# Kernel optimization log

Hardware: AMD Instinct MI355X
Metric: run time of the kernel (lower is better)

Reference implementation:

```python
import jax, jax.numpy as jnp
import numpy as np

N, S, B, E = 32768, 1024, 32, 262144   # nodes, nodes-per-graph, graphs, edges
C, H, L = 128, 4, 4                    # hidden, heads, layers
ND, ED, PE = 64, 16, 16                # node_dim, edge_dim, pe_dim
DH = C // H
LN_EPS = 1e-5


def _mlp2(h, w1, b1, w2, b2, act=jax.nn.relu):
    # mlp(ch_in, ch_out, hidden, num_hidden_layers=1): Linear -> act -> Linear (dropout = identity at inference)
    return act(h @ w1 + b1) @ w2 + b2


def _layer_norm(h, g, b):
    mu = jnp.mean(h, axis=-1, keepdims=True)
    var = jnp.var(h, axis=-1, keepdims=True)
    return (h - mu) * jax.lax.rsqrt(var + LN_EPS) * g + b


def setup_inputs() -> dict:
    key = jax.random.key(0)
    ks = iter(jax.random.split(key, 64))
    def nrm(shape, scale=0.05):
        return jax.random.normal(next(ks), shape, jnp.float32) * scale
    x = jax.random.normal(next(ks), (N, ND), jnp.float32)
    lap_pe = jax.random.normal(next(ks), (N, PE), jnp.float32)
    edge_attr = jax.random.normal(next(ks), (E, ED), jnp.float32)
    # edges within graphs: each graph occupies a contiguous block of S nodes
    g = jax.random.randint(next(ks), (E,), 0, B)
    src = g * S + jax.random.randint(next(ks), (E,), 0, S)
    dst = g * S + jax.random.randint(next(ks), (E,), 0, S)
    edge_index = jnp.stack([src, dst]).astype(jnp.int32)
    batch = (jnp.arange(N) // S).astype(jnp.int32)
    inp = dict(x=x, edge_index=edge_index, batch=batch, edge_attr=edge_attr, lap_pe=lap_pe)
    inp.update(
        node_w1=nrm((ND + PE, C)), node_b1=jnp.zeros((C,)), node_w2=nrm((C, C)), node_b2=jnp.zeros((C,)),
        edge_w1=nrm((ED, C)), edge_b1=jnp.zeros((C,)), edge_w2=nrm((C, C)), edge_b2=jnp.zeros((C,)),
        eps=jnp.zeros((L,)),
        gin_w1=nrm((L, C, C)), gin_b1=jnp.zeros((L, C)), gin_w2=nrm((L, C, C)), gin_b2=jnp.zeros((L, C)),
        elin_w=nrm((L, C, C)), elin_b=jnp.zeros((L, C)),
        attn_qkv_w=nrm((L, C, 3 * C)), attn_qkv_b=jnp.zeros((L, 3 * C)),
        attn_out_w=nrm((L, C, C)), attn_out_b=jnp.zeros((L, C)),
        mlp_w1=nrm((L, C, 2 * C)), mlp_b1=jnp.zeros((L, 2 * C)),
        mlp_w2=nrm((L, 2 * C, C)), mlp_b2=jnp.zeros((L, C)),
        ln1_g=jnp.ones((L, C)), ln1_b=jnp.zeros((L, C)),
        ln2_g=jnp.ones((L, C)), ln2_b=jnp.zeros((L, C)),
        ln3_g=jnp.ones((L, C)), ln3_b=jnp.zeros((L, C)),
        post_w1=nrm((C, C)), post_b1=jnp.zeros((C,)), post_w2=nrm((C, C)), post_b2=jnp.zeros((C,)),
        ro_w1=nrm((C, C)), ro_b1=jnp.zeros((C,)), ro_w2=nrm((C, 1)), ro_b2=jnp.zeros((1,)),
    )
    return inp


def reference(x, edge_index, batch, edge_attr, lap_pe,
              node_w1, node_b1, node_w2, node_b2,
              edge_w1, edge_b1, edge_w2, edge_b2,
              eps, gin_w1, gin_b1, gin_w2, gin_b2, elin_w, elin_b,
              attn_qkv_w, attn_qkv_b, attn_out_w, attn_out_b,
              mlp_w1, mlp_b1, mlp_w2, mlp_b2,
              ln1_g, ln1_b, ln2_g, ln2_b, ln3_g, ln3_b,
              post_w1, post_b1, post_w2, post_b2,
              ro_w1, ro_b1, ro_w2, ro_b2):
    src, dst = edge_index[0], edge_index[1]
    x = jnp.concatenate([x, lap_pe], axis=-1)
    x = _mlp2(x, node_w1, node_b1, node_w2, node_b2)
    e = _mlp2(edge_attr, edge_w1, edge_b1, edge_w2, edge_b2)
    scale = 1.0 / np.sqrt(DH)
    for i in range(L):
        # --- local GINEConv: nn((1+eps)*x_i + sum_j relu(x_j + lin(e_ij))) ---
        m = jax.nn.relu(x[src] + e @ elin_w[i] + elin_b[i])           # [E, C]
        agg = jax.ops.segment_sum(m, dst, num_segments=N)             # [N, C]
        hl = _mlp2((1.0 + eps[i]) * x + agg, gin_w1[i], gin_b1[i], gin_w2[i], gin_b2[i])
        hl = _layer_norm(hl + x, ln1_g[i], ln1_b[i])
        # --- global multihead attention over dense per-graph batch (equal sizes => reshape) ---
        xd = x.reshape(B, S, C)
        q, k, v = jnp.split(xd @ attn_qkv_w[i] + attn_qkv_b[i], 3, axis=-1)
        q = q.reshape(B, S, H, DH).transpose(0, 2, 1, 3)              # [B,H,S,DH]
        k = k.reshape(B, S, H, DH).transpose(0, 2, 1, 3)
        v = v.reshape(B, S, H, DH).transpose(0, 2, 1, 3)
        att = jax.nn.softmax(jnp.einsum('bhqd,bhkd->bhqk', q, k) * scale, axis=-1)
        o = jnp.einsum('bhqk,bhkd->bhqd', att, v).transpose(0, 2, 1, 3).reshape(B, S, C)
        ha = (o @ attn_out_w[i] + attn_out_b[i]).reshape(N, C)
        ha = _layer_norm(ha + x, ln2_g[i], ln2_b[i])
        # --- combine + FFN (act='gelu') + norm3, then outer residual ---
        out = hl + ha
        out = out + _mlp2(out, mlp_w1[i], mlp_b1[i], mlp_w2[i], mlp_b2[i], act=jax.nn.gelu)
        h = _layer_norm(out, ln3_g[i], ln3_b[i])
        x = x + h
    x = x + _mlp2(x, post_w1, post_b1, post_w2, post_b2)
    sums = jax.ops.segment_sum(x, batch, num_segments=B)
    cnt = jax.ops.segment_sum(jnp.ones((N, 1), x.dtype), batch, num_segments=B)
    gmean = sums / cnt
    return _mlp2(gmean, ro_w1, ro_b1, ro_w2, ro_b2)                   # [B, 1]
```

## Files before the change

### kernel.cpp

```cpp
#include <hip/hip_runtime.h>
#include <math.h>

namespace {

constexpr int N_  = 32768;
constexpr int S_  = 1024;
constexpr int B_  = 32;
constexpr int E_  = 262144;
constexpr int C_  = 128;
constexpr int ND_ = 64;
constexpr int PE_ = 16;
constexpr int ED_ = 16;
constexpr float LNE = 1e-5f;

typedef __attribute__((ext_vector_type(8))) short short8;
typedef __attribute__((ext_vector_type(4))) float floatx4;

__device__ inline float gelu_tanh(float v) {
  const float c = 0.7978845608028654f;
  return 0.5f * v * (1.0f + tanhf(c * (v + 0.044715f * v * v * v)));
}

__device__ inline unsigned short f2bf_u(float f) {
  unsigned u = __float_as_uint(f);
  u += 0x7fff + ((u >> 16) & 1);
  return (unsigned short)(u >> 16);
}

__device__ inline float bf2f(unsigned short v) {
  return __uint_as_float(((unsigned)v) << 16);
}

__device__ inline float block_sum128(float v, float* red, int t) {
  red[t] = v;
  __syncthreads();
#pragma unroll
  for (int off = 64; off > 0; off >>= 1) {
    if (t < off) red[t] += red[t + off];
    __syncthreads();
  }
  float r = red[0];
  __syncthreads();
  return r;
}

__global__ void k_zero(float4* __restrict__ p, int n4) {
  int i = blockIdx.x * 256 + threadIdx.x;
  if (i < n4) p[i] = make_float4(0.f, 0.f, 0.f, 0.f);
}

__global__ void k_count(const int* __restrict__ dst, int* __restrict__ hist) {
  int e = blockIdx.x * 256 + threadIdx.x;
  if (e < E_) atomicAdd(&hist[dst[e]], 1);
}

__global__ __launch_bounds__(1024) void k_scan(int* __restrict__ hist, int* __restrict__ binStart) {
  __shared__ int sums[1024];
  int t = threadIdx.x;
  int base = t * 32;
  int loc[32];
  int s = 0;
#pragma unroll
  for (int i = 0; i < 32; ++i) { loc[i] = s; s += hist[base + i]; }
  sums[t] = s;
  __syncthreads();
  for (int off = 1; off < 1024; off <<= 1) {
    int v = (t >= off) ? sums[t - off] : 0;
    __syncthreads();
    sums[t] += v;
    __syncthreads();
  }
  int excl = sums[t] - s;
#pragma unroll
  for (int i = 0; i < 32; ++i) {
    int v = excl + loc[i];
    binStart[base + i] = v;
    hist[base + i] = v;
  }
  if (t == 1023) binStart[32768] = sums[1023];
}

__global__ void k_scatter(const int* __restrict__ dst, int* __restrict__ cursor,
                          int* __restrict__ perm) {
  int e = blockIdx.x * 256 + threadIdx.x;
  if (e < E_) {
    int p = atomicAdd(&cursor[dst[e]], 1);
    perm[p] = e;
  }
}

__global__ void k_gather_edges(const float* __restrict__ ea, const int* __restrict__ src,
                               const int* __restrict__ dst, const int* __restrict__ perm,
                               float* __restrict__ ea_s, int* __restrict__ src_s,
                               int* __restrict__ dst_s) {
  int p4 = blockIdx.x * 256 + threadIdx.x;
  int p = p4 >> 2, c4 = p4 & 3;
  int e = perm[p];
  ((float4*)(ea_s + (size_t)p * ED_))[c4] = ((const float4*)(ea + (size_t)e * ED_))[c4];
  if (c4 == 0) { src_s[p] = src[e]; dst_s[p] = dst[e]; }
}

__global__ void k_fuse_w(const float* __restrict__ w2, const float* __restrict__ b2,
                         const float* __restrict__ elin_w, const float* __restrict__ elin_b,
                         unsigned short* __restrict__ fw2t, float* __restrict__ fb2) {
  int t = threadIdx.x;
  int bid = blockIdx.x;
  int layer = bid / (C_ + 1);
  int k = bid % (C_ + 1);
  const float* el = elin_w + (size_t)layer * C_ * C_;
  if (k < C_) {
    float a = 0.0f;
    for (int m = 0; m < C_; ++m) a += w2[k * C_ + m] * el[m * C_ + t];
    fw2t[(size_t)layer * C_ * C_ + t * C_ + k] = f2bf_u(a);
  } else {
    float a = elin_b[layer * C_ + t];
    for (int m = 0; m < C_; ++m) a += b2[m] * el[m * C_ + t];
    fb2[layer * C_ + t] = a;
  }
}

__global__ void k_prep_ew1(const float* __restrict__ ew1, unsigned short* __restrict__ ew1t) {
  int n = blockIdx.x;
  int k = threadIdx.x;
  ew1t[n * 32 + k] = (k < ED_) ? f2bf_u(ew1[k * C_ + n]) : (unsigned short)0;
}

__global__ void k_prep(const float* __restrict__ gin_w1, const float* __restrict__ gin_w2,
                       const float* __restrict__ aqkv_w, const float* __restrict__ aout_w,
                       const float* __restrict__ mlp_w1, const float* __restrict__ mlp_w2,
                       unsigned short* __restrict__ wt) {
  int t = threadIdx.x;
  int bid = blockIdx.x;
  int l = bid / 1152;
  int r = bid % 1152;
  unsigned short* base = wt + (size_t)l * 163840;
  if (r < 128) {
    base[r * 128 + t] = f2bf_u(gin_w1[(size_t)l * 16384 + t * 128 + r]);
  } else if (r < 256) {
    int n = r - 128;
    base[16384 + n * 128 + t] = f2bf_u(gin_w2[(size_t)l * 16384 + t * 128 + n]);
  } else if (r < 640) {
    int n = r - 256;
    base[32768 + n * 128 + t] = f2bf_u(aqkv_w[(size_t)l * 49152 + t * 384 + n]);
  } else if (r < 768) {
    int n = r - 640;
    base[81920 + n * 128 + t] = f2bf_u(aout_w[(size_t)l * 16384 + t * 128 + n]);
  } else if (r < 1024) {
    int n = r - 768;
    base[98304 + n * 128 + t] = f2bf_u(mlp_w1[(size_t)l * 32768 + t * 256 + n]);
  } else {
    int n = r - 1024;
    base[131072 + n * 256 + t]       = f2bf_u(mlp_w2[(size_t)l * 32768 + t * 128 + n]);
    base[131072 + n * 256 + 128 + t] = f2bf_u(mlp_w2[(size_t)l * 32768 + (t + 128) * 128 + n]);
  }
}

__global__ void k_node_enc(const float* __restrict__ xin, const float* __restrict__ pe,
                           const float* __restrict__ w1, const float* __restrict__ b1,
                           const float* __restrict__ w2, const float* __restrict__ b2,
                           float* __restrict__ xout) {
  __shared__ float inL[4][80];
  __shared__ float hidL[4][C_];
  int t = threadIdx.x;
  int row0 = blockIdx.x * 4;
#pragma unroll
  for (int r = 0; r < 4; ++r) {
    int row = row0 + r;
    if (t < ND_) inL[r][t] = xin[(size_t)row * ND_ + t];
    else if (t < 80) inL[r][t] = pe[(size_t)row * PE_ + (t - ND_)];
  }
  __syncthreads();
  float acc[4];
  float bb = b1[t];
#pragma unroll
  for (int r = 0; r < 4; ++r) acc[r] = bb;
  for (int k = 0; k < 80; ++k) {
    float wv = w1[k * C_ + t];
#pragma unroll
    for (int r = 0; r < 4; ++r) acc[r] += inL[r][k] * wv;
  }
#pragma unroll
  for (int r = 0; r < 4; ++r) hidL[r][t] = fmaxf(acc[r], 0.0f);
  __syncthreads();
  float bb2 = b2[t];
#pragma unroll
  for (int r = 0; r < 4; ++r) acc[r] = bb2;
  for (int k = 0; k < C_; ++k) {
    float wv = w2[k * C_ + t];
#pragma unroll
    for (int r = 0; r < 4; ++r) acc[r] += hidL[r][k] * wv;
  }
#pragma unroll
  for (int r = 0; r < 4; ++r) xout[(size_t)(row0 + r) * C_ + t] = acc[r];
}

__global__ __launch_bounds__(256) void k_edge_mfma(
    const float* __restrict__ ea_s, const float* __restrict__ x,
    const int* __restrict__ src_s, const int* __restrict__ dst_s,
    const unsigned short* __restrict__ ew1t, const float* __restrict__ eb1,
    const unsigned short* __restrict__ fw2t, const float* __restrict__ fb2,
    float* __restrict__ agg) {
  __shared__ unsigned short eaL[64][40];
  __shared__ unsigned short buf[64][136];
  __shared__ int srcL[64], dstL[64];
  int tid = threadIdx.x;
  int e0 = blockIdx.x * 64;

  if (tid < 64) { srcL[tid] = src_s[e0 + tid]; dstL[tid] = dst_s[e0 + tid]; }
  {
    int r = tid >> 2, c4 = tid & 3;
    float4 v = ((const float4*)(ea_s + (size_t)(e0 + r) * ED_))[c4];
    ushort4 u;
    u.x = f2bf_u(v.x); u.y = f2bf_u(v.y); u.z = f2bf_u(v.z); u.w = f2bf_u(v.w);
    *(ushort4*)&eaL[r][c4 * 4] = u;
    ushort4 z4 = {0, 0, 0, 0};
    *(ushort4*)&eaL[r][16 + c4 * 4] = z4;
  }
  __syncthreads();

  int lane = tid & 63;
  int w = tid >> 6;
  int li = lane & 15;
  int quad = lane >> 4;
  int r0 = w * 16;

  short8 aE = *(const short8*)&eaL[r0 + li][quad * 8];
#pragma unroll
  for (int t8 = 0; t8 < 8; ++t8) {
    short8 bE = *(const short8*)(ew1t + (size_t)(t8 * 16 + li) * 32 + quad * 8);
    floatx4 z = {0.f, 0.f, 0.f, 0.f};
    floatx4 h = __builtin_amdgcn_mfma_f32_16x16x32_bf16(aE, bE, z, 0, 0, 0);
    float bv = eb1[t8 * 16 + li];
#pragma unroll
    for (int reg = 0; reg < 4; ++reg)
      buf[r0 + quad * 4 + reg][t8 * 16 + li] = f2bf_u(fmaxf(h[reg] + bv, 0.f));
  }
  __syncthreads();

  short8 aK[4];
#pragma unroll
  for (int k4 = 0; k4 < 4; ++k4)
    aK[k4] = *(const short8*)&buf[r0 + li][k4 * 32 + quad * 8];
  __syncthreads();

  float fbv[8];
#pragma unroll
  for (int t8 = 0; t8 < 8; ++t8) fbv[t8] = fb2[t8 * 16 + li];

#pragma unroll
  for (int t8 = 0; t8 < 8; ++t8) {
    floatx4 acc = {0.f, 0.f, 0.f, 0.f};
    const unsigned short* bp = fw2t + (size_t)(t8 * 16 + li) * C_ + quad * 8;
#pragma unroll
    for (int k4 = 0; k4 < 4; ++k4) {
      short8 bf = *(const short8*)(bp + k4 * 32);
      acc = __builtin_amdgcn_mfma_f32_16x16x32_bf16(aK[k4], bf, acc, 0, 0, 0);
    }
    int n = t8 * 16 + li;
#pragma unroll
    for (int reg = 0; reg < 4; ++reg) {
      int cr = r0 + quad * 4 + reg;
      float v = fmaxf(acc[reg] + fbv[t8] + x[(size_t)srcL[cr] * C_ + n], 0.0f);
      buf[cr][n] = f2bf_u(v);
    }
  }
  __syncthreads();

  {
    int col = tid & 127;
    int rbase = (tid >> 7) * 32;
    float run = bf2f(buf[rbase][col]);
    int cur = dstL[rbase];
    for (int r = 1; r < 32; ++r) {
      int rr = rbase + r;
      int d = dstL[rr];
      float v = bf2f(buf[rr][col]);
      if (d != cur) {
        atomicAdd(&agg[(size_t)cur * C_ + col], run);
        run = v; cur = d;
      } else {
        run += v;
      }
    }
    atomicAdd(&agg[(size_t)cur * C_ + col], run);
  }
}

__global__ __launch_bounds__(256) void k_gin_mfma(
    const float* __restrict__ x, const float* __restrict__ agg,
    const unsigned short* __restrict__ w1t, const float* __restrict__ b1,
    const unsigned short* __restrict__ w2t, const float* __restrict__ b2,
    const float* __restrict__ g, const float* __restrict__ bln,
    const float* __restrict__ epsarr, int layer, float* __restrict__ hl) {
  __shared__ unsigned short inL[64][136];
  __shared__ unsigned short hidL[64][136];
  int tid = threadIdx.x;
  int row0 = blockIdx.x * 64;
  float epsv = 1.0f + epsarr[layer];
#pragma unroll
  for (int i = 0; i < 8; ++i) {
    int p = i * 256 + tid;
    int r = p >> 5, c4 = p & 31;
    float4 xa = *(const float4*)(x + (size_t)(row0 + r) * C_ + c4 * 4);
    float4 ag = *(const float4*)(agg + (size_t)(row0 + r) * C_ + c4 * 4);
    ushort4 u;
    u.x = f2bf_u(epsv * xa.x + ag.x);
    u.y = f2bf_u(epsv * xa.y + ag.y);
    u.z = f2bf_u(epsv * xa.z + ag.z);
    u.w = f2bf_u(epsv * xa.w + ag.w);
    *(ushort4*)&inL[r][c4 * 4] = u;
  }
  __syncthreads();
  int lane = tid & 63, w = tid >> 6, li = lane & 15, quad = lane >> 4;
  int r0 = w * 16;

  short8 aK[4];
#pragma unroll
  for (int k4 = 0; k4 < 4; ++k4) aK[k4] = *(const short8*)&inL[r0 + li][k4 * 32 + quad * 8];
  floatx4 acc[8];
#pragma unroll
  for (int t8 = 0; t8 < 8; ++t8) acc[t8] = (floatx4){0.f, 0.f, 0.f, 0.f};
#pragma unroll
  for (int t8 = 0; t8 < 8; ++t8) {
    const unsigned short* bp = w1t + (size_t)(t8 * 16 + li) * 128 + quad * 8;
#pragma unroll
    for (int k4 = 0; k4 < 4; ++k4) {
      short8 bf = *(const short8*)(bp + k4 * 32);
      acc[t8] = __builtin_amdgcn_mfma_f32_16x16x32_bf16(aK[k4], bf, acc[t8], 0, 0, 0);
    }
  }
#pragma unroll
  for (int t8 = 0; t8 < 8; ++t8) {
    float bv = b1[t8 * 16 + li];
#pragma unroll
    for (int reg = 0; reg < 4; ++reg)
      hidL[r0 + quad * 4 + reg][t8 * 16 + li] = f2bf_u(fmaxf(acc[t8][reg] + bv, 0.f));
  }
  short8 aK2[4];
#pragma unroll
  for (int k4 = 0; k4 < 4; ++k4) aK2[k4] = *(const short8*)&hidL[r0 + li][k4 * 32 + quad * 8];
  floatx4 acc2[8];
#pragma unroll
  for (int t8 = 0; t8 < 8; ++t8) acc2[t8] = (floatx4){0.f, 0.f, 0.f, 0.f};
#pragma unroll
  for (int t8 = 0; t8 < 8; ++t8) {
    const unsigned short* bp = w2t + (size_t)(t8 * 16 + li) * 128 + quad * 8;
#pragma unroll
    for (int k4 = 0; k4 < 4; ++k4) {
      short8 bf = *(const short8*)(bp + k4 * 32);
      acc2[t8] = __builtin_amdgcn_mfma_f32_16x16x32_bf16(aK2[k4], bf, acc2[t8], 0, 0, 0);
    }
  }
  float gv[8], blv[8], b2v[8];
#pragma unroll
  for (int t8 = 0; t8 < 8; ++t8) {
    int col = t8 * 16 + li;
    gv[t8] = g[col]; blv[t8] = bln[col]; b2v[t8] = b2[col];
  }
#pragma unroll
  for (int reg = 0; reg < 4; ++reg) {
    int row = row0 + r0 + quad * 4 + reg;
    float v[8], s = 0.f, s2 = 0.f;
#pragma unroll
    for (int t8 = 0; t8 < 8; ++t8) {
      float xv = x[(size_t)row * C_ + t8 * 16 + li];
      v[t8] = acc2[t8][reg] + b2v[t8] + xv;
      s += v[t8]; s2 += v[t8] * v[t8];
    }
#pragma unroll
    for (int m = 1; m <= 8; m <<= 1) { s += __shfl_xor(s, m); s2 += __shfl_xor(s2, m); }
    float mu = s * (1.0f / C_);
    float var = s2 * (1.0f / C_) - mu * mu;
    float inv = rsqrtf(var + LNE);
#pragma unroll
    for (int t8 = 0; t8 < 8; ++t8)
      hl[(size_t)row * C_ + t8 * 16 + li] = (v[t8] - mu) * inv * gv[t8] + blv[t8];
  }
}

__global__ __launch_bounds__(256) void k_qkv_mfma(
    const float* __restrict__ x, const unsigned short* __restrict__ qkvt,
    const float* __restrict__ b, unsigned short* __restrict__ qkvb) {
  __shared__ unsigned short inL[64][136];
  int tid = threadIdx.x;
  int row0 = blockIdx.x * 64;
#pragma unroll
  for (int i = 0; i < 8; ++i) {
    int p = i * 256 + tid;
    int r = p >> 5, c4 = p & 31;
    float4 xa = *(const float4*)(x + (size_t)(row0 + r) * C_ + c4 * 4);
    ushort4 u;
    u.x = f2bf_u(xa.x); u.y = f2bf_u(xa.y); u.z = f2bf_u(xa.z); u.w = f2bf_u(xa.w);
    *(ushort4*)&inL[r][c4 * 4] = u;
  }
  __syncthreads();
  int lane = tid & 63, w = tid >> 6, li = lane & 15, quad = lane >> 4;
  int r0 = w * 16;
  short8 aK[4];
#pragma unroll
  for (int k4 = 0; k4 < 4; ++k4) aK[k4] = *(const short8*)&inL[r0 + li][k4 * 32 + quad * 8];
  floatx4 acc[24];
#pragma unroll
  for (int t8 = 0; t8 < 24; ++t8) acc[t8] = (floatx4){0.f, 0.f, 0.f, 0.f};
#pragma unroll
  for (int t8 = 0; t8 < 24; ++t8) {
    const unsigned short* bp = qkvt + (size_t)(t8 * 16 + li) * 128 + quad * 8;
#pragma unroll
    for (int k4 = 0; k4 < 4; ++k4) {
      short8 bf = *(const short8*)(bp + k4 * 32);
      acc[t8] = __builtin_amdgcn_mfma_f32_16x16x32_bf16(aK[k4], bf, acc[t8], 0, 0, 0);
    }
  }
#pragma unroll
  for (int t8 = 0; t8 < 24; ++t8) {
    int col = t8 * 16 + li;
    float bv = b[col];
#pragma unroll
    for (int reg = 0; reg < 4; ++reg) {
      int row = row0 + r0 + quad * 4 + reg;
      qkvb[(size_t)row * 384 + col] = f2bf_u(acc[t8][reg] + bv);
    }
  }
}

__global__ __launch_bounds__(256) void k_attn_mfma(const unsigned short* __restrict__ qkvb,
                                                   float* __restrict__ attno) {
  __shared__ unsigned short kL[2][32][40];
  __shared__ unsigned short vT[2][32][40];
  __shared__ unsigned short pL[4][16][40];
  int tid = threadIdx.x;
  int lane = tid & 63;
  int w = tid >> 6;
  int li = lane & 15;
  int quad = lane >> 4;
  int bid = blockIdx.x;
  int b = (bid & 7) * 4 + ((bid >> 3) & 3);
  int rest = bid >> 5;
  int h = rest & 3;
  int qt = rest >> 2;
  int qbase = b * S_ + qt * 64 + w * 16;

  short8 qA = *(const short8*)(qkvb + (size_t)(qbase + li) * 384 + h * 32 + quad * 8);

  floatx4 o0 = {0.f, 0.f, 0.f, 0.f}, o1 = {0.f, 0.f, 0.f, 0.f};
  float lsum[4] = {0.f, 0.f, 0.f, 0.f};
  const float scale = 0.17677669529663687f;

  int half = tid >> 7;
  int tt = tid & 127;
  int j = tt >> 2;
  int seg = tt & 3;
  int vcol = (((j >> 3) ^ seg) & 3) * 8 + (j & 7);
  int vg0 = ((quad ^ (li >> 3)) & 3) * 8;
  int vg1 = ((quad ^ (2 + (li >> 3))) & 3) * 8;

  for (int kc = 0; kc < 32; ++kc) {
    int buf = kc & 1;
    {
      int node = b * S_ + kc * 32 + j;
      const unsigned short* p = qkvb + (size_t)node * 384 + (half ? 256 : 128) + h * 32 + seg * 8;
      short8 val = *(const short8*)p;
      if (half == 0) {
        *(short8*)&kL[buf][j][seg * 8] = val;
      } else {
#pragma unroll
        for (int i = 0; i < 8; ++i) vT[buf][seg * 8 + i][vcol] = (unsigned short)val[i];
      }
    }
    __syncthreads();
    short8 kB0 = *(const short8*)&kL[buf][li][quad * 8];
    short8 kB1 = *(const short8*)&kL[buf][16 + li][quad * 8];
    floatx4 z = {0.f, 0.f, 0.f, 0.f};
    floatx4 s0 = __builtin_amdgcn_mfma_f32_16x16x32_bf16(qA, kB0, z, 0, 0, 0);
    floatx4 s1 = __builtin_amdgcn_mfma_f32_16x16x32_bf16(qA, kB1, z, 0, 0, 0);
#pragma unroll
    for (int r = 0; r < 4; ++r) {
      float p0 = __expf(s0[r] * scale);
      float p1 = __expf(s1[r] * scale);
      lsum[r] += p0 + p1;
      pL[w][quad * 4 + r][li] = f2bf_u(p0);
      pL[w][quad * 4 + r][16 + li] = f2bf_u(p1);
    }
    short8 pA  = *(const short8*)&pL[w][li][quad * 8];
    short8 vB0 = *(const short8*)&vT[buf][li][vg0];
    short8 vB1 = *(const short8*)&vT[buf][16 + li][vg1];
    o0 = __builtin_amdgcn_mfma_f32_16x16x32_bf16(pA, vB0, o0, 0, 0, 0);
    o1 = __builtin_amdgcn_mfma_f32_16x16x32_bf16(pA, vB1, o1, 0, 0, 0);
  }
#pragma unroll
  for (int r = 0; r < 4; ++r) {
    float l = lsum[r];
#pragma unroll
    for (int msk = 1; msk <= 8; msk <<= 1) l += __shfl_xor(l, msk);
    float inv = 1.0f / l;
    size_t row = (size_t)(qbase + quad * 4 + r);
    attno[row * C_ + h * 32 + li] = o0[r] * inv;
    attno[row * C_ + h * 32 + 16 + li] = o1[r] * inv;
  }
}

__global__ __launch_bounds__(256) void k_attnout_mfma(
    const float* __restrict__ attno, const float* __restrict__ x,
    const unsigned short* __restrict__ wt, const float* __restrict__ b,
    const float* __restrict__ g, const float* __restrict__ bln,
    float* __restrict__ ha) {
  __shared__ unsigned short inL[64][136];
  int tid = threadIdx.x;
  int row0 = blockIdx.x * 64;
#pragma unroll
  for (int i = 0; i < 8; ++i) {
    int p = i * 256 + tid;
    int r = p >> 5, c4 = p & 31;
    float4 xa = *(const float4*)(attno + (size_t)(row0 + r) * C_ + c4 * 4);
    ushort4 u;
    u.x = f2bf_u(xa.x); u.y = f2bf_u(xa.y); u.z = f2bf_u(xa.z); u.w = f2bf_u(xa.w);
    *(ushort4*)&inL[r][c4 * 4] = u;
  }
  __syncthreads();
  int lane = tid & 63, w = tid >> 6, li = lane & 15, quad = lane >> 4;
  int r0 = w * 16;
  short8 aK[4];
#pragma unroll
  for (int k4 = 0; k4 < 4; ++k4) aK[k4] = *(const short8*)&inL[r0 + li][k4 * 32 + quad * 8];
  floatx4 acc[8];
#pragma unroll
  for (int t8 = 0; t8 < 8; ++t8) acc[t8] = (floatx4){0.f, 0.f, 0.f, 0.f};
#pragma unroll
  for (int t8 = 0; t8 < 8; ++t8) {
    const unsigned short* bp = wt + (size_t)(t8 * 16 + li) * 128 + quad * 8;
#pragma unroll
    for (int k4 = 0; k4 < 4; ++k4) {
      short8 bf = *(const short8*)(bp + k4 * 32);
      acc[t8] = __builtin_amdgcn_mfma_f32_16x16x32_bf16(aK[k4], bf, acc[t8], 0, 0, 0);
    }
  }
  float gv[8], blv[8], bv[8];
#pragma unroll
  for (int t8 = 0; t8 < 8; ++t8) {
    int col = t8 * 16 + li;
    gv[t8] = g[col]; blv[t8] = bln[col]; bv[t8] = b[col];
  }
#pragma unroll
  for (int reg = 0; reg < 4; ++reg) {
    int row = row0 + r0 + quad * 4 + reg;
    float v[8], s = 0.f, s2 = 0.f;
#pragma unroll
    for (int t8 = 0; t8 < 8; ++t8) {
      float xv = x[(size_t)row * C_ + t8 * 16 + li];
      v[t8] = acc[t8][reg] + bv[t8] + xv;
      s += v[t8]; s2 += v[t8] * v[t8];
    }
#pragma unroll
    for (int m = 1; m <= 8; m <<= 1) { s += __shfl_xor(s, m); s2 += __shfl_xor(s2, m); }
    float mu = s * (1.0f / C_);
    float var = s2 * (1.0f / C_) - mu * mu;
    float inv = rsqrtf(var + LNE);
#pragma unroll
    for (int t8 = 0; t8 < 8; ++t8)
      ha[(size_t)row * C_ + t8 * 16 + li] = (v[t8] - mu) * inv * gv[t8] + blv[t8];
  }
}

__global__ __launch_bounds__(256) void k_ffn_mfma(
    const float* __restrict__ hl, const float* __restrict__ ha,
    float* __restrict__ x,
    const unsigned short* __restrict__ w1t, const float* __restrict__ b1,
    const unsigned short* __restrict__ w2t, const float* __restrict__ b2,
    const float* __restrict__ g, const float* __restrict__ bln) {
  __shared__ unsigned short inL[64][136];
  __shared__ unsigned short hidL[64][264];
  int tid = threadIdx.x;
  int row0 = blockIdx.x * 64;
#pragma unroll
  for (int i = 0; i < 8; ++i) {
    int p = i * 256 + tid;
    int r = p >> 5, c4 = p & 31;
    float4 a = *(const float4*)(hl + (size_t)(row0 + r) * C_ + c4 * 4);
    float4 bq = *(const float4*)(ha + (size_t)(row0 + r) * C_ + c4 * 4);
    ushort4 u;
    u.x = f2bf_u(a.x + bq.x); u.y = f2bf_u(a.y + bq.y);
    u.z = f2bf_u(a.z + bq.z); u.w = f2bf_u(a.w + bq.w);
    *(ushort4*)&inL[r][c4 * 4] = u;
  }
  __syncthreads();
  int lane = tid & 63, w = tid >> 6, li = lane & 15, quad = lane >> 4;
  int r0 = w * 16;
  short8 aK[4];
#pragma unroll
  for (int k4 = 0; k4 < 4; ++k4) aK[k4] = *(const short8*)&inL[r0 + li][k4 * 32 + quad * 8];
  floatx4 acc1[16];
#pragma unroll
  for (int t8 = 0; t8 < 16; ++t8) acc1[t8] = (floatx4){0.f, 0.f, 0.f, 0.f};
#pragma unroll
  for (int t8 = 0; t8 < 16; ++t8) {
    const unsigned short* bp = w1t + (size_t)(t8 * 16 + li) * 128 + quad * 8;
#pragma unroll
    for (int k4 = 0; k4 < 4; ++k4) {
      short8 bf = *(const short8*)(bp + k4 * 32);
      acc1[t8] = __builtin_amdgcn_mfma_f32_16x16x32_bf16(aK[k4], bf, acc1[t8], 0, 0, 0);
    }
  }
#pragma unroll
  for (int t8 = 0; t8 < 16; ++t8) {
    float bv = b1[t8 * 16 + li];
#pragma unroll
    for (int reg = 0; reg < 4; ++reg)
      hidL[r0 + quad * 4 + reg][t8 * 16 + li] = f2bf_u(gelu_tanh(acc1[t8][reg] + bv));
  }
  short8 aK2[8];
#pragma unroll
  for (int k4 = 0; k4 < 8; ++k4) aK2[k4] = *(const short8*)&hidL[r0 + li][k4 * 32 + quad * 8];
  floatx4 acc2[8];
#pragma unroll
  for (int t8 = 0; t8 < 8; ++t8) acc2[t8] = (floatx4){0.f, 0.f, 0.f, 0.f};
#pragma unroll
  for (int t8 = 0; t8 < 8; ++t8) {
    const unsigned short* bp = w2t + (size_t)(t8 * 16 + li) * 256 + quad * 8;
#pragma unroll
    for (int k4 = 0; k4 < 8; ++k4) {
      short8 bf = *(const short8*)(bp + k4 * 32);
      acc2[t8] = __builtin_amdgcn_mfma_f32_16x16x32_bf16(aK2[k4], bf, acc2[t8], 0, 0, 0);
    }
  }
  float gv[8], blv[8], b2v[8];
#pragma unroll
  for (int t8 = 0; t8 < 8; ++t8) {
    int col = t8 * 16 + li;
    gv[t8] = g[col]; blv[t8] = bln[col]; b2v[t8] = b2[col];
  }
#pragma unroll
  for (int reg = 0; reg < 4; ++reg) {
    int row = row0 + r0 + quad * 4 + reg;
    float v[8], s = 0.f, s2 = 0.f;
#pragma unroll
    for (int t8 = 0; t8 < 8; ++t8) {
      size_t idx = (size_t)row * C_ + t8 * 16 + li;
      float outv = hl[idx] + ha[idx];
      v[t8] = acc2[t8][reg] + b2v[t8] + outv;
      s += v[t8]; s2 += v[t8] * v[t8];
    }
#pragma unroll
    for (int m = 1; m <= 8; m <<= 1) { s += __shfl_xor(s, m); s2 += __shfl_xor(s2, m); }
    float mu = s * (1.0f / C_);
    float var = s2 * (1.0f / C_) - mu * mu;
    float inv = rsqrtf(var + LNE);
#pragma unroll
    for (int t8 = 0; t8 < 8; ++t8) {
      size_t idx = (size_t)row * C_ + t8 * 16 + li;
      x[idx] = x[idx] + (v[t8] - mu) * inv * gv[t8] + blv[t8];
    }
  }
}

__global__ void k_post(float* __restrict__ x,
                       const float* __restrict__ w1, const float* __restrict__ b1,
                       const float* __restrict__ w2, const float* __restrict__ b2) {
  __shared__ float inL[4][C_];
  __shared__ float hidL[4][C_];
  int t = threadIdx.x;
  int row0 = blockIdx.x * 4;
  float xv[4];
#pragma unroll
  for (int r = 0; r < 4; ++r) {
    size_t idx = (size_t)(row0 + r) * C_ + t;
    xv[r] = x[idx];
    inL[r][t] = xv[r];
  }
  __syncthreads();
  float acc[4];
  float bb = b1[t];
#pragma unroll
  for (int r = 0; r < 4; ++r) acc[r] = bb;
  for (int k = 0; k < C_; ++k) {
    float wv = w1[k * C_ + t];
#pragma unroll
    for (int r = 0; r < 4; ++r) acc[r] += inL[r][k] * wv;
  }
#pragma unroll
  for (int r = 0; r < 4; ++r) hidL[r][t] = fmaxf(acc[r], 0.0f);
  __syncthreads();
  float bb2 = b2[t];
#pragma unroll
  for (int r = 0; r < 4; ++r) acc[r] = bb2;
  for (int k = 0; k < C_; ++k) {
    float wv = w2[k * C_ + t];
#pragma unroll
    for (int r = 0; r < 4; ++r) acc[r] += hidL[r][k] * wv;
  }
#pragma unroll
  for (int r = 0; r < 4; ++r) {
    size_t idx = (size_t)(row0 + r) * C_ + t;
    x[idx] = xv[r] + acc[r];
  }
}

__global__ void k_pool(const float* __restrict__ x, float* __restrict__ gmean) {
  int t = threadIdx.x;
  int b = blockIdx.x;
  float s = 0.0f;
  for (int sidx = 0; sidx < S_; ++sidx) s += x[((size_t)b * S_ + sidx) * C_ + t];
  gmean[b * C_ + t] = s * (1.0f / S_);
}

__global__ void k_readout(const float* __restrict__ gmean,
                          const float* __restrict__ w1, const float* __restrict__ b1,
                          const float* __restrict__ w2, const float* __restrict__ b2,
                          float* __restrict__ out) {
  __shared__ float gL[C_];
  __shared__ float red[C_];
  int t = threadIdx.x;
  int b = blockIdx.x;
  gL[t] = gmean[b * C_ + t];
  __syncthreads();
  float acc = b1[t];
  for (int k = 0; k < C_; ++k) acc += gL[k] * w1[k * C_ + t];
  float hid = fmaxf(acc, 0.0f);
  float part = hid * w2[t];
  float tot = block_sum128(part, red, t);
  if (t == 0) out[b] = tot + b2[0];
}

}

extern "C" void kernel_launch(void* const* d_in, const int* in_sizes, int n_in,
                              void* d_out, int out_size, void* d_ws, size_t ws_size,
                              hipStream_t stream) {
  const float* in_x      = (const float*)d_in[0];
  const int*   edge_idx  = (const int*)d_in[1];
  const float* edge_attr = (const float*)d_in[3];
  const float* lap_pe    = (const float*)d_in[4];
  const float* node_w1 = (const float*)d_in[5];
  const float* node_b1 = (const float*)d_in[6];
  const float* node_w2 = (const float*)d_in[7];
  const float* node_b2 = (const float*)d_in[8];
  const float* edge_w1 = (const float*)d_in[9];
  const float* edge_b1 = (const float*)d_in[10];
  const float* edge_w2 = (const float*)d_in[11];
  const float* edge_b2 = (const float*)d_in[12];
  const float* eps     = (const float*)d_in[13];
  const float* gin_w1  = (const float*)d_in[14];
  const float* gin_b1  = (const float*)d_in[15];
  const float* gin_w2  = (const float*)d_in[16];
  const float* gin_b2  = (const float*)d_in[17];
  const float* elin_w  = (const float*)d_in[18];
  const float* elin_b  = (const float*)d_in[19];
  const float* aqkv_w  = (const float*)d_in[20];
  const float* aqkv_b  = (const float*)d_in[21];
  const float* aout_w  = (const float*)d_in[22];
  const float* aout_b  = (const float*)d_in[23];
  const float* mlp_w1  = (const float*)d_in[24];
  const float* mlp_b1  = (const float*)d_in[25];
  const float* mlp_w2  = (const float*)d_in[26];
  const float* mlp_b2  = (const float*)d_in[27];
  const float* ln1_g   = (const float*)d_in[28];
  const float* ln1_b   = (const float*)d_in[29];
  const float* ln2_g   = (const float*)d_in[30];
  const float* ln2_b   = (const float*)d_in[31];
  const float* ln3_g   = (const float*)d_in[32];
  const float* ln3_b   = (const float*)d_in[33];
  const float* post_w1 = (const float*)d_in[34];
  const float* post_b1 = (const float*)d_in[35];
  const float* post_w2 = (const float*)d_in[36];
  const float* post_b2 = (const float*)d_in[37];
  const float* ro_w1   = (const float*)d_in[38];
  const float* ro_b1   = (const float*)d_in[39];
  const float* ro_w2   = (const float*)d_in[40];
  const float* ro_b2   = (const float*)d_in[41];

  const int* src = edge_idx;
  const int* dst = edge_idx + E_;

  float* ws = (float*)d_ws;
  float* x     = ws;
  float* region2 = x + (size_t)N_ * C_;
  float* agg   = region2;
  unsigned short* qkvb = (unsigned short*)region2;
  float* hl    = region2 + (size_t)N_ * 192;
  float* attno = hl + (size_t)N_ * C_;
  float* ha    = attno;
  float* fb2   = attno + (size_t)N_ * C_;
  unsigned short* fw2tb = (unsigned short*)(fb2 + 4 * C_);
  unsigned short* wt = fw2tb + (size_t)4 * C_ * C_;
  unsigned short* ew1tb = wt + 655360;
  float* ea_s  = (float*)(ew1tb + 4096);
  int* src_s   = (int*)(ea_s + (size_t)E_ * ED_);
  int* dst_s   = src_s + E_;
  int* hist    = dst_s + E_;
  int* binStart = hist + 32768;
  int* perm    = binStart + 32769;
  float* gmean = hl;

  float* out = (float*)d_out;

  dim3 blk(128);
  const size_t LWS = 163840;

  k_fuse_w<<<4 * (C_ + 1), blk, 0, stream>>>(edge_w2, edge_b2, elin_w, elin_b, fw2tb, fb2);
  k_prep<<<4 * 1152, blk, 0, stream>>>(gin_w1, gin_w2, aqkv_w, aout_w, mlp_w1, mlp_w2, wt);
  k_prep_ew1<<<128, 32, 0, stream>>>(edge_w1, ew1tb);
  k_zero<<<(32768 / 4 + 255) / 256, 256, 0, stream>>>((float4*)hist, 32768 / 4);
  k_count<<<E_ / 256, 256, 0, stream>>>(dst, hist);
  k_scan<<<1, 1024, 0, stream>>>(hist, binStart);
  k_scatter<<<E_ / 256, 256, 0, stream>>>(dst, hist, perm);
  k_gather_edges<<<E_ * 4 / 256, 256, 0, stream>>>(edge_attr, src, dst, perm,
                                                   ea_s, src_s, dst_s);
  k_node_enc<<<N_ / 4, blk, 0, stream>>>(in_x, lap_pe, node_w1, node_b1, node_w2, node_b2, x);

  for (int i = 0; i < 4; ++i) {
    const unsigned short* wl = wt + (size_t)i * LWS;
    k_zero<<<(N_ * C_ / 4 + 255) / 256, 256, 0, stream>>>((float4*)agg, N_ * C_ / 4);
    k_edge_mfma<<<E_ / 64, 256, 0, stream>>>(ea_s, x, src_s, dst_s,
                                             ew1tb, edge_b1,
                                             fw2tb + (size_t)i * C_ * C_, fb2 + i * C_, agg);
    k_gin_mfma<<<N_ / 64, 256, 0, stream>>>(x, agg,
                                            wl + 0, gin_b1 + i * C_,
                                            wl + 16384, gin_b2 + i * C_,
                                            ln1_g + i * C_, ln1_b + i * C_, eps, i, hl);
    k_qkv_mfma<<<N_ / 64, 256, 0, stream>>>(x, wl + 32768, aqkv_b + i * 384, qkvb);
    k_attn_mfma<<<B_ * 4 * 16, 256, 0, stream>>>(qkvb, attno);
    k_attnout_mfma<<<N_ / 64, 256, 0, stream>>>(attno, x,
                                                wl + 81920, aout_b + i * C_,
                                                ln2_g + i * C_, ln2_b + i * C_, ha);
    k_ffn_mfma<<<N_ / 64, 256, 0, stream>>>(hl, ha, x,
                                            wl + 98304, mlp_b1 + i * 256,
                                            wl + 131072, mlp_b2 + i * C_,
                                            ln3_g + i * C_, ln3_b + i * C_);
  }

  k_post<<<N_ / 4, blk, 0, stream>>>(x, post_w1, post_b1, post_w2, post_b2);
  k_pool<<<B_, blk, 0, stream>>>(x, gmean);
  k_readout<<<B_, blk, 0, stream>>>(gmean, ro_w1, ro_b1, ro_w2, ro_b2, out);
}
```

Baseline: 1.511 ms.

## Fuse GIN with QKV projection and attention-out with FFN; prefetch K/V in attention

Merges the GIN MLP kernel with the QKV projection so x is read once per row tile, and merges the attention output projection plus LayerNorm with the FFN so the intermediate ha/out tensors stay in registers and LDS. The attention kernel now loads the next K/V chunk into registers before computing on the current one. Buffer layout is reshuffled so agg aliases the attention output region, since qkvb and agg are now live at the same time. The fused kernels use more LDS and registers per block, which may lower occupancy.

New measurement: 1.412 ms. -6.6%, faster.

```diff
diff --git a/kernel.cpp b/kernel.cpp
--- a/kernel.cpp
+++ b/kernel.cpp
@@ -286,14 +286,16 @@
   }
 }
 
-__global__ __launch_bounds__(256) void k_gin_mfma(
+__global__ __launch_bounds__(256) void k_ginqkv(
     const float* __restrict__ x, const float* __restrict__ agg,
     const unsigned short* __restrict__ w1t, const float* __restrict__ b1,
     const unsigned short* __restrict__ w2t, const float* __restrict__ b2,
     const float* __restrict__ g, const float* __restrict__ bln,
-    const float* __restrict__ epsarr, int layer, float* __restrict__ hl) {
+    const float* __restrict__ epsarr, int layer, float* __restrict__ hl,
+    const unsigned short* __restrict__ qkvt, const float* __restrict__ qb,
+    unsigned short* __restrict__ qkvb) {
   __shared__ unsigned short inL[64][136];
-  __shared__ unsigned short hidL[64][136];
+  __shared__ unsigned short xbL[64][136];
   int tid = threadIdx.x;
   int row0 = blockIdx.x * 64;
   float epsv = 1.0f + epsarr[layer];
@@ -303,6 +305,9 @@
     int r = p >> 5, c4 = p & 31;
     float4 xa = *(const float4*)(x + (size_t)(row0 + r) * C_ + c4 * 4);
     float4 ag = *(const float4*)(agg + (size_t)(row0 + r) * C_ + c4 * 4);
+    ushort4 ux;
+    ux.x = f2bf_u(xa.x); ux.y = f2bf_u(xa.y); ux.z = f2bf_u(xa.z); ux.w = f2bf_u(xa.w);
+    *(ushort4*)&xbL[r][c4 * 4] = ux;
     ushort4 u;
     u.x = f2bf_u(epsv * xa.x + ag.x);
     u.y = f2bf_u(epsv * xa.y + ag.y);
@@ -317,28 +322,23 @@
   short8 aK[4];
 #pragma unroll
   for (int k4 = 0; k4 < 4; ++k4) aK[k4] = *(const short8*)&inL[r0 + li][k4 * 32 + quad * 8];
-  floatx4 acc[8];
-#pragma unroll
-  for (int t8 = 0; t8 < 8; ++t8) acc[t8] = (floatx4){0.f, 0.f, 0.f, 0.f};
-#pragma unroll
-  for (int t8 = 0; t8 < 8; ++t8) {
+#pragma unroll
+  for (int t8 = 0; t8 < 8; ++t8) {
+    floatx4 acc = {0.f, 0.f, 0.f, 0.f};
     const unsigned short* bp = w1t + (size_t)(t8 * 16 + li) * 128 + quad * 8;
 #pragma unroll
     for (int k4 = 0; k4 < 4; ++k4) {
       short8 bf = *(const short8*)(bp + k4 * 32);
-      acc[t8] = __builtin_amdgcn_mfma_f32_16x16x32_bf16(aK[k4], bf, acc[t8], 0, 0, 0);
-    }
-  }
-#pragma unroll
-  for (int t8 = 0; t8 < 8; ++t8) {
+      acc = __builtin_amdgcn_mfma_f32_16x16x32_bf16(aK[k4], bf, acc, 0, 0, 0);
+    }
     float bv = b1[t8 * 16 + li];
 #pragma unroll
     for (int reg = 0; reg < 4; ++reg)
-      hidL[r0 + quad * 4 + reg][t8 * 16 + li] = f2bf_u(fmaxf(acc[t8][reg] + bv, 0.f));
+      inL[r0 + quad * 4 + reg][t8 * 16 + li] = f2bf_u(fmaxf(acc[reg] + bv, 0.f));
   }
   short8 aK2[4];
 #pragma unroll
-  for (int k4 = 0; k4 < 4; ++k4) aK2[k4] = *(const short8*)&hidL[r0 + li][k4 * 32 + quad * 8];
+  for (int k4 = 0; k4 < 4; ++k4) aK2[k4] = *(const short8*)&inL[r0 + li][k4 * 32 + quad * 8];
   floatx4 acc2[8];
 #pragma unroll
   for (int t8 = 0; t8 < 8; ++t8) acc2[t8] = (floatx4){0.f, 0.f, 0.f, 0.f};
@@ -376,49 +376,25 @@
     for (int t8 = 0; t8 < 8; ++t8)
       hl[(size_t)row * C_ + t8 * 16 + li] = (v[t8] - mu) * inv * gv[t8] + blv[t8];
   }
-}
-
-__global__ __launch_bounds__(256) void k_qkv_mfma(
-    const float* __restrict__ x, const unsigned short* __restrict__ qkvt,
-    const float* __restrict__ b, unsigned short* __restrict__ qkvb) {
-  __shared__ unsigned short inL[64][136];
-  int tid = threadIdx.x;
-  int row0 = blockIdx.x * 64;
-#pragma unroll
-  for (int i = 0; i < 8; ++i) {
-    int p = i * 256 + tid;
-    int r = p >> 5, c4 = p & 31;
-    float4 xa = *(const float4*)(x + (size_t)(row0 + r) * C_ + c4 * 4);
-    ushort4 u;
-    u.x = f2bf_u(xa.x); u.y = f2bf_u(xa.y); u.z = f2bf_u(xa.z); u.w = f2bf_u(xa.w);
-    *(ushort4*)&inL[r][c4 * 4] = u;
-  }
-  __syncthreads();
-  int lane = tid & 63, w = tid >> 6, li = lane & 15, quad = lane >> 4;
-  int r0 = w * 16;
-  short8 aK[4];
-#pragma unroll
-  for (int k4 = 0; k4 < 4; ++k4) aK[k4] = *(const short8*)&inL[r0 + li][k4 * 32 + quad * 8];
-  floatx4 acc[24];
-#pragma unroll
-  for (int t8 = 0; t8 < 24; ++t8) acc[t8] = (floatx4){0.f, 0.f, 0.f, 0.f};
+
+  short8 aQ[4];
+#pragma unroll
+  for (int k4 = 0; k4 < 4; ++k4) aQ[k4] = *(const short8*)&xbL[r0 + li][k4 * 32 + quad * 8];
 #pragma unroll
   for (int t8 = 0; t8 < 24; ++t8) {
+    floatx4 acc = {0.f, 0.f, 0.f, 0.f};
     const unsigned short* bp = qkvt + (size_t)(t8 * 16 + li) * 128 + quad * 8;
 #pragma unroll
     for (int k4 = 0; k4 < 4; ++k4) {
       short8 bf = *(const short8*)(bp + k4 * 32);
-      acc[t8] = __builtin_amdgcn_mfma_f32_16x16x32_bf16(aK[k4], bf, acc[t8], 0, 0, 0);
-    }
-  }
-#pragma unroll
-  for (int t8 = 0; t8 < 24; ++t8) {
+      acc = __builtin_amdgcn_mfma_f32_16x16x32_bf16(aQ[k4], bf, acc, 0, 0, 0);
+    }
     int col = t8 * 16 + li;
-    float bv = b[col];
+    float bv = qb[col];
 #pragma unroll
     for (int reg = 0; reg < 4; ++reg) {
       int row = row0 + r0 + quad * 4 + reg;
-      qkvb[(size_t)row * 384 + col] = f2bf_u(acc[t8][reg] + bv);
+      qkvb[(size_t)row * 384 + col] = f2bf_u(acc[reg] + bv);
     }
   }
 }
@@ -454,20 +430,21 @@
   int vg0 = ((quad ^ (li >> 3)) & 3) * 8;
   int vg1 = ((quad ^ (2 + (li >> 3))) & 3) * 8;
 
+  const unsigned short* pbase = qkvb + (half ? 256 : 128) + h * 32 + seg * 8;
+
+  short8 val = *(const short8*)(pbase + (size_t)(b * S_ + 0 * 32 + j) * 384);
+
   for (int kc = 0; kc < 32; ++kc) {
     int buf = kc & 1;
-    {
-      int node = b * S_ + kc * 32 + j;
-      const unsigned short* p = qkvb + (size_t)node * 384 + (half ? 256 : 128) + h * 32 + seg * 8;
-      short8 val = *(const short8*)p;
-      if (half == 0) {
-        *(short8*)&kL[buf][j][seg * 8] = val;
-      } else {
-#pragma unroll
-        for (int i = 0; i < 8; ++i) vT[buf][seg * 8 + i][vcol] = (unsigned short)val[i];
-      }
+    if (half == 0) {
+      *(short8*)&kL[buf][j][seg * 8] = val;
+    } else {
+#pragma unroll
+      for (int i = 0; i < 8; ++i) vT[buf][seg * 8 + i][vcol] = (unsigned short)val[i];
     }
     __syncthreads();
+    if (kc < 31)
+      val = *(const short8*)(pbase + (size_t)(b * S_ + (kc + 1) * 32 + j) * 384);
     short8 kB0 = *(const short8*)&kL[buf][li][quad * 8];
     short8 kB1 = *(const short8*)&kL[buf][16 + li][quad * 8];
     floatx4 z = {0.f, 0.f, 0.f, 0.f};
@@ -499,12 +476,16 @@
   }
 }
 
-__global__ __launch_bounds__(256) void k_attnout_mfma(
-    const float* __restrict__ attno, const float* __restrict__ x,
-    const unsigned short* __restrict__ wt, const float* __restrict__ b,
-    const float* __restrict__ g, const float* __restrict__ bln,
-    float* __restrict__ ha) {
+__global__ __launch_bounds__(256) void k_aoffn(
+    const float* __restrict__ attno, float* __restrict__ x,
+    const float* __restrict__ hl,
+    const unsigned short* __restrict__ aot, const float* __restrict__ ab,
+    const float* __restrict__ g2, const float* __restrict__ bl2,
+    const unsigned short* __restrict__ w1t, const float* __restrict__ b1,
+    const unsigned short* __restrict__ w2t, const float* __restrict__ b2,
+    const float* __restrict__ g3, const float* __restrict__ bl3) {
   __shared__ unsigned short inL[64][136];
+  __shared__ unsigned short hidL[64][264];
   int tid = threadIdx.x;
   int row0 = blockIdx.x * 64;
 #pragma unroll
@@ -519,6 +500,7 @@
   __syncthreads();
   int lane = tid & 63, w = tid >> 6, li = lane & 15, quad = lane >> 4;
   int r0 = w * 16;
+
   short8 aK[4];
 #pragma unroll
   for (int k4 = 0; k4 < 4; ++k4) aK[k4] = *(const short8*)&inL[r0 + li][k4 * 32 + quad * 8];
@@ -527,19 +509,20 @@
   for (int t8 = 0; t8 < 8; ++t8) acc[t8] = (floatx4){0.f, 0.f, 0.f, 0.f};
 #pragma unroll
   for (int t8 = 0; t8 < 8; ++t8) {
-    const unsigned short* bp = wt + (size_t)(t8 * 16 + li) * 128 + quad * 8;
+    const unsigned short* bp = aot + (size_t)(t8 * 16 + li) * 128 + quad * 8;
 #pragma unroll
     for (int k4 = 0; k4 < 4; ++k4) {
       short8 bf = *(const short8*)(bp + k4 * 32);
       acc[t8] = __builtin_amdgcn_mfma_f32_16x16x32_bf16(aK[k4], bf, acc[t8], 0, 0, 0);
     }
   }
-  float gv[8], blv[8], bv[8];
+  float g2v[8], bl2v[8], abv[8];
 #pragma unroll
   for (int t8 = 0; t8 < 8; ++t8) {
     int col = t8 * 16 + li;
-    gv[t8] = g[col]; blv[t8] = bln[col]; bv[t8] = b[col];
-  }
+    g2v[t8] = g2[col]; bl2v[t8] = bl2[col]; abv[t8] = ab[col];
+  }
+  float outv[8][4];
 #pragma unroll
   for (int reg = 0; reg < 4; ++reg) {
     int row = row0 + r0 + quad * 4 + reg;
@@ -547,7 +530,7 @@
 #pragma unroll
     for (int t8 = 0; t8 < 8; ++t8) {
       float xv = x[(size_t)row * C_ + t8 * 16 + li];
-      v[t8] = acc[t8][reg] + bv[t8] + xv;
+      v[t8] = acc[t8][reg] + abv[t8] + xv;
       s += v[t8]; s2 += v[t8] * v[t8];
     }
 #pragma unroll
@@ -556,60 +539,35 @@
     float var = s2 * (1.0f / C_) - mu * mu;
     float inv = rsqrtf(var + LNE);
 #pragma unroll
-    for (int t8 = 0; t8 < 8; ++t8)
-      ha[(size_t)row * C_ + t8 * 16 + li] = (v[t8] - mu) * inv * gv[t8] + blv[t8];
-  }
-}
-
-__global__ __launch_bounds__(256) void k_ffn_mfma(
-    const float* __restrict__ hl, const float* __restrict__ ha,
-    float* __restrict__ x,
-    const unsigned short* __restrict__ w1t, const float* __restrict__ b1,
-    const unsigned short* __restrict__ w2t, const float* __restrict__ b2,
-    const float* __restrict__ g, const float* __restrict__ bln) {
-  __shared__ unsigned short inL[64][136];
-  __shared__ unsigned short hidL[64][264];
-  int tid = threadIdx.x;
-  int row0 = blockIdx.x * 64;
-#pragma unroll
-  for (int i = 0; i < 8; ++i) {
-    int p = i * 256 + tid;
-    int r = p >> 5, c4 = p & 31;
-    float4 a = *(const float4*)(hl + (size_t)(row0 + r) * C_ + c4 * 4);
-    float4 bq = *(const float4*)(ha + (size_t)(row0 + r) * C_ + c4 * 4);
-    ushort4 u;
-    u.x = f2bf_u(a.x + bq.x); u.y = f2bf_u(a.y + bq.y);
-    u.z = f2bf_u(a.z + bq.z); u.w = f2bf_u(a.w + bq.w);
-    *(ushort4*)&inL[r][c4 * 4] = u;
-  }
-  __syncthreads();
-  int lane = tid & 63, w = tid >> 6, li = lane & 15, quad = lane >> 4;
-  int r0 = w * 16;
-  short8 aK[4];
-#pragma unroll
-  for (int k4 = 0; k4 < 4; ++k4) aK[k4] = *(const short8*)&inL[r0 + li][k4 * 32 + quad * 8];
-  floatx4 acc1[16];
-#pragma unroll
-  for (int t8 = 0; t8 < 16; ++t8) acc1[t8] = (floatx4){0.f, 0.f, 0.f, 0.f};
+    for (int t8 = 0; t8 < 8; ++t8) {
+      int col = t8 * 16 + li;
+      float ha = (v[t8] - mu) * inv * g2v[t8] + bl2v[t8];
+      float ov = hl[(size_t)row * C_ + col] + ha;
+      outv[t8][reg] = ov;
+      inL[r0 + quad * 4 + reg][col] = f2bf_u(ov);
+    }
+  }
+
+  short8 aK2[4];
+#pragma unroll
+  for (int k4 = 0; k4 < 4; ++k4) aK2[k4] = *(const short8*)&inL[r0 + li][k4 * 32 + quad * 8];
 #pragma unroll
   for (int t8 = 0; t8 < 16; ++t8) {
+    floatx4 a1 = {0.f, 0.f, 0.f, 0.f};
     const unsigned short* bp = w1t + (size_t)(t8 * 16 + li) * 128 + quad * 8;
 #pragma unroll
     for (int k4 = 0; k4 < 4; ++k4) {
       short8 bf = *(const short8*)(bp + k4 * 32);
-      acc1[t8] = __builtin_amdgcn_mfma_f32_16x16x32_bf16(aK[k4], bf, acc1[t8], 0, 0, 0);
-    }
-  }
-#pragma unroll
-  for (int t8 = 0; t8 < 16; ++t8) {
+      a1 = __builtin_amdgcn_mfma_f32_16x16x32_bf16(aK2[k4], bf, a1, 0, 0, 0);
+    }
     float bv = b1[t8 * 16 + li];
 #pragma unroll
     for (int reg = 0; reg < 4; ++reg)
-      hidL[r0 + quad * 4 + reg][t8 * 16 + li] = f2bf_u(gelu_tanh(acc1[t8][reg] + bv));
-  }
-  short8 aK2[8];
-#pragma unroll
-  for (int k4 = 0; k4 < 8; ++k4) aK2[k4] = *(const short8*)&hidL[r0 + li][k4 * 32 + quad * 8];
+      hidL[r0 + quad * 4 + reg][t8 * 16 + li] = f2bf_u(gelu_tanh(a1[reg] + bv));
+  }
+  short8 aK3[8];
+#pragma unroll
+  for (int k4 = 0; k4 < 8; ++k4) aK3[k4] = *(const short8*)&hidL[r0 + li][k4 * 32 + quad * 8];
   floatx4 acc2[8];
 #pragma unroll
   for (int t8 = 0; t8 < 8; ++t8) acc2[t8] = (floatx4){0.f, 0.f, 0.f, 0.f};
@@ -619,14 +577,14 @@
 #pragma unroll
     for (int k4 = 0; k4 < 8; ++k4) {
       short8 bf = *(const short8*)(bp + k4 * 32);
-      acc2[t8] = __builtin_amdgcn_mfma_f32_16x16x32_bf16(aK2[k4], bf, acc2[t8], 0, 0, 0);
-    }
-  }
-  float gv[8], blv[8], b2v[8];
+      acc2[t8] = __builtin_amdgcn_mfma_f32_16x16x32_bf16(aK3[k4], bf, acc2[t8], 0, 0, 0);
+    }
+  }
+  float g3v[8], bl3v[8], b2v[8];
 #pragma unroll
   for (int t8 = 0; t8 < 8; ++t8) {
     int col = t8 * 16 + li;
-    gv[t8] = g[col]; blv[t8] = bln[col]; b2v[t8] = b2[col];
+    g3v[t8] = g3[col]; bl3v[t8] = bl3[col]; b2v[t8] = b2[col];
   }
 #pragma unroll
   for (int reg = 0; reg < 4; ++reg) {
@@ -634,9 +592,7 @@
     float v[8], s = 0.f, s2 = 0.f;
 #pragma unroll
     for (int t8 = 0; t8 < 8; ++t8) {
-      size_t idx = (size_t)row * C_ + t8 * 16 + li;
-      float outv = hl[idx] + ha[idx];
-      v[t8] = acc2[t8][reg] + b2v[t8] + outv;
+      v[t8] = acc2[t8][reg] + b2v[t8] + outv[t8][reg];
       s += v[t8]; s2 += v[t8] * v[t8];
     }
 #pragma unroll
@@ -647,7 +603,7 @@
 #pragma unroll
     for (int t8 = 0; t8 < 8; ++t8) {
       size_t idx = (size_t)row * C_ + t8 * 16 + li;
-      x[idx] = x[idx] + (v[t8] - mu) * inv * gv[t8] + blv[t8];
+      x[idx] = x[idx] + (v[t8] - mu) * inv * g3v[t8] + bl3v[t8];
     }
   }
 }
@@ -772,12 +728,10 @@
 
   float* ws = (float*)d_ws;
   float* x     = ws;
-  float* region2 = x + (size_t)N_ * C_;
-  float* agg   = region2;
-  unsigned short* qkvb = (unsigned short*)region2;
-  float* hl    = region2 + (size_t)N_ * 192;
+  unsigned short* qkvb = (unsigned short*)(x + (size_t)N_ * C_);
+  float* hl    = x + (size_t)N_ * C_ + (size_t)N_ * 192;
   float* attno = hl + (size_t)N_ * C_;
-  float* ha    = attno;
+  float* agg   = attno;
   float* fb2   = attno + (size_t)N_ * C_;
   unsigned short* fw2tb = (unsigned short*)(fb2 + 4 * C_);
   unsigned short* wt = fw2tb + (size_t)4 * C_ * C_;
@@ -812,19 +766,18 @@
     k_edge_mfma<<<E_ / 64, 256, 0, stream>>>(ea_s, x, src_s, dst_s,
                                              ew1tb, edge_b1,
                                              fw2tb + (size_t)i * C_ * C_, fb2 + i * C_, agg);
-    k_gin_mfma<<<N_ / 64, 256, 0, stream>>>(x, agg,
-                                            wl + 0, gin_b1 + i * C_,
-                                            wl + 16384, gin_b2 + i * C_,
-                                            ln1_g + i * C_, ln1_b + i * C_, eps, i, hl);
-    k_qkv_mfma<<<N_ / 64, 256, 0, stream>>>(x, wl + 32768, aqkv_b + i * 384, qkvb);
+    k_ginqkv<<<N_ / 64, 256, 0, stream>>>(x, agg,
+                                          wl + 0, gin_b1 + i * C_,
+                                          wl + 16384, gin_b2 + i * C_,
+                                          ln1_g + i * C_, ln1_b + i * C_, eps, i, hl,
+                                          wl + 32768, aqkv_b + i * 384, qkvb);
     k_attn_mfma<<<B_ * 4 * 16, 256, 0, stream>>>(qkvb, attno);
-    k_attnout_mfma<<<N_ / 64, 256, 0, stream>>>(attno, x,
-                                                wl + 81920, aout_b + i * C_,
-                                                ln2_g + i * C_, ln2_b + i * C_, ha);
-    k_ffn_mfma<<<N_ / 64, 256, 0, stream>>>(hl, ha, x,
-                                            wl + 98304, mlp_b1 + i * 256,
-                                            wl + 131072, mlp_b2 + i * C_,
-                                            ln3_g + i * C_, ln3_b + i * C_);
+    k_aoffn<<<N_ / 64, 256, 0, stream>>>(attno, x, hl,
+                                         wl + 81920, aout_b + i * C_,
+                                         ln2_g + i * C_, ln2_b + i * C_,
+                                         wl + 98304, mlp_b1 + i * 256,
+                                         wl + 131072, mlp_b2 + i * C_,
+                                         ln3_g + i * C_, ln3_b + i * C_);
   }
 
   k_post<<<N_ / 4, blk, 0, stream>>>(x, post_w1, post_b1, post_w2, post_b2);
```
